# Performance work log

Measured on AMD Instinct MI355X. Metric: run time of the kernel, lower is better.

Reference implementation:

```python
import jax, jax.numpy as jnp
import numpy as np

N_FFT = 4096
HOP = 1024
WIN = 300          # wiener_win_len (frames per independent Wiener chunk)
EPS = 1e-10
SCALE_FACTOR = 10.0


def hann(n):
    # torch.hann_window (periodic)
    return 0.5 * (1.0 - jnp.cos(2.0 * jnp.pi * jnp.arange(n) / n))


def stft(x, window):
    # x: (N, C, T) -> complex (N, C, B, F), center=True, reflect pad, onesided
    pad = N_FFT // 2
    xp = jnp.pad(x, ((0, 0), (0, 0), (pad, pad)), mode='reflect')
    n_frames = 1 + (xp.shape[-1] - N_FFT) // HOP
    idx = jnp.arange(n_frames)[:, None] * HOP + jnp.arange(N_FFT)[None, :]
    frames = xp[..., idx] * window                      # (N,C,F,n_fft)
    spec = jnp.fft.rfft(frames, axis=-1)                # (N,C,F,B)
    return jnp.swapaxes(spec, -1, -2)                   # (N,C,B,F)


def istft(spec, window, length):
    # spec: (..., B, F) complex -> (..., length) real; center=True inverse
    frames = jnp.fft.irfft(jnp.swapaxes(spec, -1, -2), n=N_FFT, axis=-1) * window
    n_frames = frames.shape[-2]
    out_len = N_FFT + HOP * (n_frames - 1)
    idx = jnp.arange(n_frames)[:, None] * HOP + jnp.arange(N_FFT)[None, :]
    out = jnp.zeros(frames.shape[:-2] + (out_len,), frames.dtype).at[..., idx].add(frames)
    wsum = jnp.zeros((out_len,), frames.dtype).at[idx].add(
        jnp.broadcast_to(window ** 2, idx.shape))
    out = out / jnp.where(wsum > 1e-11, wsum, 1.0)
    pad = N_FFT // 2
    return out[..., pad:pad + length]


def wiener_chunk(v, x, niter):
    # openunmix.filtering.wiener (softmask=False, residual=False) on one chunk.
    # v: (T, B, C, S) real target magnitudes; x: (T, B, C) complex mix STFT.
    phase = jnp.exp(1j * jnp.angle(x))                  # mixture phase init
    y = (v * phase[..., None]).astype(jnp.complex64)    # (T,B,C,S)
    max_abs = jnp.maximum(1.0, jnp.max(jnp.abs(x)) / SCALE_FACTOR)
    x = x / max_abs
    y = y / max_abs
    C = x.shape[-1]
    reg = np.sqrt(EPS) * jnp.eye(C, dtype=jnp.complex64)
    for _ in range(niter):  # expectation_maximization, one pass per iter
        psd = jnp.mean(jnp.abs(y) ** 2, axis=2)         # (T,B,S) channel-avg PSD
        # spatial covariance per bin/source, normalized by eps + sum_t psd
        R = jnp.einsum('tbcs,tbds->bcds', y, jnp.conj(y))
        R = R / (EPS + jnp.sum(psd, axis=0))[:, None, None, :]
        Cxx = reg + jnp.einsum('tbs,bcds->tbcd', psd.astype(jnp.complex64), R)
        inv = jnp.linalg.inv(Cxx)                       # (T,B,C,C)
        gain = jnp.einsum('bacs,tbcd->tbads', R, inv) * psd[:, :, None, None, :]
        y = jnp.einsum('tbacs,tbc->tbas', gain, x)      # (T,B,C,S)
    return y * max_abs


def setup_inputs() -> dict:
    key = jax.random.key(0)
    k1, k2 = jax.random.split(key)
    audio = jax.random.normal(k1, (2, 2, 613376), dtype=jnp.float32)
    W = jax.random.normal(k2, (4, 2049), dtype=jnp.float32)  # per-target per-bin mask logits
    return {'audio': audio, 'W': W, 'niter': 1}


def reference(audio, W, niter):
    window = hann(N_FFT).astype(audio.dtype)
    mix = stft(audio, window)                           # (N,C,B,F) complex
    X = jnp.abs(mix)                                    # ComplexNorm power=1
    # target models (stand-in: per-bin sigmoid masks); input detached as in torch
    Xd = jax.lax.stop_gradient(X)
    masks = jax.nn.sigmoid(W)                           # (S,B)
    specs = Xd[..., None] * jnp.transpose(masks)[None, None, :, None, :]  # (N,C,B,F,S)
    v = jnp.transpose(specs, (0, 3, 2, 1, 4))           # (N,F,B,C,S)
    xm = jnp.transpose(mix, (0, 3, 2, 1))               # (N,F,B,C)
    N, F, B, C = xm.shape
    S = v.shape[-1]
    n_chunks = F // WIN
    vc = v.reshape(N, n_chunks, WIN, B, C, S)
    xc = xm.reshape(N, n_chunks, WIN, B, C)
    wfun = lambda vv, xx: wiener_chunk(vv, xx, niter)
    yc = jax.vmap(jax.vmap(wfun))(vc, xc)               # (N,chunks,T,B,C,S)
    y = yc.reshape(N, F, B, C, S)
    y = jnp.transpose(y, (0, 4, 3, 2, 1))               # (N,S,C,B,F)
    estimates = istft(y, window, audio.shape[-1])       # (N,S,C,T)
    return estimates
```

## Files before the change

### kernel.cpp

```cpp
#include <hip/hip_runtime.h>
#include <math.h>

#define TLEN 613376
#define OLEN 617472
#define NFR  600
#define NB   2049
#define PI_F  3.14159265358979323846f
#define PI2_F 6.28318530717958647693f
#define PHYS(i) ((i) + ((i) >> 4))

__device__ __forceinline__ float winf(int j) {
  return 0.5f - 0.5f * __cosf(1.5339807878856412e-3f * (float)j);
}

__device__ __forceinline__ float reflect_load(const float* __restrict__ x, int pos) {
  int k = pos - 2048;
  if (k < 0) k = -k;
  else if (k >= TLEN) k = 2 * TLEN - 2 - k;
  return x[k];
}

__device__ __forceinline__ float2 cmul(float2 a, float2 b) {
  return make_float2(a.x * b.x - a.y * b.y, a.x * b.y + a.y * b.x);
}
__device__ __forceinline__ float2 cadd(float2 a, float2 b) { return make_float2(a.x + b.x, a.y + b.y); }
__device__ __forceinline__ float2 csub(float2 a, float2 b) { return make_float2(a.x - b.x, a.y - b.y); }
template<int SGN>
__device__ __forceinline__ float2 muli(float2 a) {
  return (SGN > 0) ? make_float2(-a.y, a.x) : make_float2(a.y, -a.x);
}

template<int SGN>
__device__ __forceinline__ void fft4(float2 v[4]) {
  float2 t0 = cadd(v[0], v[2]), t1 = csub(v[0], v[2]);
  float2 t2 = cadd(v[1], v[3]), t3 = csub(v[1], v[3]);
  float2 it3 = muli<SGN>(t3);
  v[0] = cadd(t0, t2); v[2] = csub(t0, t2);
  v[1] = cadd(t1, it3); v[3] = csub(t1, it3);
}

template<int SGN>
__device__ __forceinline__ void fft8(float2 v[8]) {
  const float C = 0.70710678118654752440f;
  const float s = (SGN > 0) ? 1.0f : -1.0f;
  float2 t0 = cadd(v[0], v[4]), t1 = csub(v[0], v[4]);
  float2 t2 = cadd(v[2], v[6]), t3 = csub(v[2], v[6]);
  float2 e0 = cadd(t0, t2), e2 = csub(t0, t2);
  float2 it3 = muli<SGN>(t3);
  float2 e1 = cadd(t1, it3), e3 = csub(t1, it3);
  t0 = cadd(v[1], v[5]); t1 = csub(v[1], v[5]);
  t2 = cadd(v[3], v[7]); t3 = csub(v[3], v[7]);
  float2 o0 = cadd(t0, t2), o2 = csub(t0, t2);
  it3 = muli<SGN>(t3);
  float2 o1 = cadd(t1, it3), o3 = csub(t1, it3);
  float2 o1w = make_float2(C * (o1.x - s * o1.y), C * (o1.y + s * o1.x));
  float2 o2w = muli<SGN>(o2);
  float2 o3w = make_float2(C * (-o3.x - s * o3.y), C * (-o3.y + s * o3.x));
  v[0] = cadd(e0, o0);  v[4] = csub(e0, o0);
  v[1] = cadd(e1, o1w); v[5] = csub(e1, o1w);
  v[2] = cadd(e2, o2w); v[6] = csub(e2, o2w);
  v[3] = cadd(e3, o3w); v[7] = csub(e3, o3w);
}

template<int SGN>
__device__ __forceinline__ void twiddle8(float2 v[8], float ang) {
  float sn, cs;
  __sincosf((SGN > 0) ? ang : -ang, &sn, &cs);
  float2 w1 = make_float2(cs, sn);
  float2 w = w1;
  v[1] = cmul(v[1], w);
#pragma unroll
  for (int r = 2; r < 8; ++r) { w = cmul(w, w1); v[r] = cmul(v[r], w); }
}

template<int SGN>
__device__ __forceinline__ void fft2048_mid(float2* lds, float2 v[8], int tid) {
  fft8<SGN>(v);
#pragma unroll
  for (int r = 0; r < 8; ++r) { int i = tid * 8 + r; lds[PHYS(i)] = v[r]; }
  __syncthreads();
#pragma unroll
  for (int r = 0; r < 8; ++r) v[r] = lds[PHYS(tid + 256 * r)];
  twiddle8<SGN>(v, PI2_F * (1.0f / 64.0f) * (float)(tid & 7));
  fft8<SGN>(v);
  __syncthreads();
#pragma unroll
  for (int r = 0; r < 8; ++r) { int i = ((tid >> 3) << 6) + (tid & 7) + 8 * r; lds[PHYS(i)] = v[r]; }
  __syncthreads();
#pragma unroll
  for (int r = 0; r < 8; ++r) v[r] = lds[PHYS(tid + 256 * r)];
  twiddle8<SGN>(v, PI2_F * (1.0f / 512.0f) * (float)(tid & 63));
  fft8<SGN>(v);
  __syncthreads();
#pragma unroll
  for (int r = 0; r < 8; ++r) { int i = ((tid >> 6) << 9) + (tid & 63) + 64 * r; lds[PHYS(i)] = v[r]; }
  __syncthreads();
}

template<int SGN>
__device__ __forceinline__ void fft2048_last(const float2* lds, int jj, float2 u[4]) {
#pragma unroll
  for (int r = 0; r < 4; ++r) u[r] = lds[PHYS(jj + 512 * r)];
  float sn, cs;
  float ang = PI2_F * (1.0f / 2048.0f) * (float)jj;
  __sincosf((SGN > 0) ? ang : -ang, &sn, &cs);
  float2 w1 = make_float2(cs, sn);
  float2 w2 = cmul(w1, w1);
  float2 w3 = cmul(w2, w1);
  u[1] = cmul(u[1], w1); u[2] = cmul(u[2], w2); u[3] = cmul(u[3], w3);
  fft4<SGN>(u);
}

__global__ __launch_bounds__(256, 6) void stft_kernel(const float* __restrict__ audio,
                                                      float2* __restrict__ X) {
  __shared__ float2 lds[2176];
  int bid = blockIdx.x;
  int f  = bid % NFR;
  int nc = bid / NFR;
  const float* x = audio + (size_t)nc * TLEN;
  int tid = threadIdx.x;
  int base = f * 1024;
  float2 v[8];
#pragma unroll
  for (int r = 0; r < 8; ++r) {
    int k = tid + 256 * r;
    int j0 = 2 * k;
    v[r] = make_float2(reflect_load(x, base + j0)     * winf(j0),
                       reflect_load(x, base + j0 + 1) * winf(j0 + 1));
  }
  fft2048_mid<-1>(lds, v, tid);
  fft2048_last<-1>(lds, tid,        v);
  fft2048_last<-1>(lds, tid + 256,  v + 4);
  __syncthreads();
#pragma unroll
  for (int r = 0; r < 4; ++r) lds[PHYS(tid + 512 * r)] = v[r];
#pragma unroll
  for (int r = 0; r < 4; ++r) lds[PHYS(tid + 256 + 512 * r)] = v[4 + r];
  __syncthreads();
  float2* out = X + (size_t)bid * NB;
  float sn0, cs0;
  __sincosf(-PI_F * (float)tid * (1.0f / 2048.0f), &sn0, &cs0);
  float2 ph = make_float2(cs0, sn0);
  const float2 rot = make_float2(0.92387953251128675613f, -0.38268343236508977173f);
#pragma unroll
  for (int r = 0; r < 9; ++r) {
    int k = tid + 256 * r;
    if (k <= 2048) {
      float2 Zk = lds[PHYS(k & 2047)];
      float2 Zm = lds[PHYS((2048 - k) & 2047)];
      float Ex = 0.5f * (Zk.x + Zm.x), Ey = 0.5f * (Zk.y - Zm.y);
      float Dx = 0.5f * (Zk.x - Zm.x), Dy = 0.5f * (Zk.y + Zm.y);
      float Ox = Dy, Oy = -Dx;
      out[k] = make_float2(Ex + Ox * ph.x - Oy * ph.y, Ey + Ox * ph.y + Oy * ph.x);
    }
    ph = cmul(ph, rot);
  }
}

__global__ __launch_bounds__(256) void maxred_kernel(const float2* __restrict__ X,
                                                     unsigned int* __restrict__ maxsq) {
  __shared__ unsigned int sm;
  if (threadIdx.x == 0) sm = 0u;
  __syncthreads();
  int g = blockIdx.y;
  int n = g >> 1, chunk = g & 1;
  const int len = 300 * NB;
  const float2* p0 = X + ((size_t)(n * 2 + 0) * NFR + chunk * 300) * NB;
  const float2* p1 = X + ((size_t)(n * 2 + 1) * NFR + chunk * 300) * NB;
  float l = 0.f;
  for (int i = blockIdx.x * 256 + threadIdx.x; i < len; i += 64 * 256) {
    float2 a = p0[i]; l = fmaxf(l, a.x * a.x + a.y * a.y);
    float2 b = p1[i]; l = fmaxf(l, b.x * b.x + b.y * b.y);
  }
  atomicMax(&sm, __float_as_uint(l));
  __syncthreads();
  if (threadIdx.x == 0) atomicMax(&maxsq[g], sm);
}

__global__ __launch_bounds__(256) void stats_kernel(const float2* __restrict__ X,
                                                    float* __restrict__ stats) {
  int b = blockIdx.x * 256 + threadIdx.x;
  if (b >= NB) return;
  int g = blockIdx.y;
  int n = g >> 1, chunk = g & 1;
  int t0 = blockIdx.z * 75;
  const float2* X0 = X + ((size_t)(n * 2 + 0) * NFR + chunk * 300 + t0) * NB + b;
  const float2* X1 = X + ((size_t)(n * 2 + 1) * NFR + chunk * 300 + t0) * NB + b;
  float s00 = 0.f, s11 = 0.f, sre = 0.f, sim = 0.f;
  for (int t = 0; t < 75; ++t) {
    float2 a = X0[(size_t)t * NB];
    float2 c = X1[(size_t)t * NB];
    s00 += a.x * a.x + a.y * a.y;
    s11 += c.x * c.x + c.y * c.y;
    sre += a.x * c.x + a.y * c.y;
    sim += a.y * c.x - a.x * c.y;
  }
  unsafeAtomicAdd(&stats[(size_t)(g * 4 + 0) * NB + b], s00);
  unsafeAtomicAdd(&stats[(size_t)(g * 4 + 1) * NB + b], s11);
  unsafeAtomicAdd(&stats[(size_t)(g * 4 + 2) * NB + b], sre);
  unsafeAtomicAdd(&stats[(size_t)(g * 4 + 3) * NB + b], sim);
}

__global__ __launch_bounds__(256) void alpha_kernel(const float* __restrict__ Wmask,
                                                    const float* __restrict__ stats,
                                                    const unsigned int* __restrict__ maxsq,
                                                    float* __restrict__ alpha) {
  int idx = blockIdx.x * 256 + threadIdx.x;
  if (idx >= 4 * 4 * NB) return;
  int b = idx % NB;
  int gs = idx / NB;
  int s = gs & 3;
  int g = gs >> 2;
  float ma2 = fmaxf(1.0f, __uint_as_float(maxsq[g]) * 0.01f);
  float P = 0.5f * (stats[(size_t)(g * 4 + 0) * NB + b] +
                    stats[(size_t)(g * 4 + 1) * NB + b]) / ma2;
  float mv = 1.0f / (1.0f + expf(-Wmask[s * NB + b]));
  float m2 = mv * mv;
  alpha[idx] = (m2 * m2) / (1e-10f + m2 * P);
}

__global__ __launch_bounds__(256) void wiener_kernel(const float2* __restrict__ X,
                                                     const float* __restrict__ stats,
                                                     const float* __restrict__ alpha,
                                                     const unsigned int* __restrict__ maxsq,
                                                     float2* __restrict__ Wc) {
  int idx = blockIdx.x * 256 + threadIdx.x;
  if (idx >= 4 * 300 * NB) return;
  int b = idx % NB;
  int gt = idx / NB;
  int t = gt % 300;
  int g = gt / 300;
  int n = g >> 1, chunk = g & 1;
  int f = chunk * 300 + t;
  float ma2 = fmaxf(1.0f, __uint_as_float(maxsq[g]) * 0.01f);
  float inv_ma2 = 1.0f / ma2;
  float g00 = stats[(size_t)(g * 4 + 0) * NB + b] * inv_ma2;
  float g11 = stats[(size_t)(g * 4 + 1) * NB + b] * inv_ma2;
  float gre = stats[(size_t)(g * 4 + 2) * NB + b] * inv_ma2;
  float gim = stats[(size_t)(g * 4 + 3) * NB + b] * inv_ma2;
  float K = alpha[(size_t)(g * 4 + 0) * NB + b] + alpha[(size_t)(g * 4 + 1) * NB + b] +
            alpha[(size_t)(g * 4 + 2) * NB + b] + alpha[(size_t)(g * 4 + 3) * NB + b];
  float2 x0 = X[((size_t)(n * 2 + 0) * NFR + f) * NB + b];
  float2 x1 = X[((size_t)(n * 2 + 1) * NFR + f) * NB + b];
  float ph = 0.5f * ((x0.x * x0.x + x0.y * x0.y) + (x1.x * x1.x + x1.y * x1.y)) * inv_ma2;
  float pk = ph * K;
  float M00 = 1e-5f + pk * g00;
  float M11 = 1e-5f + pk * g11;
  float Mre = pk * gre, Mim = pk * gim;
  float det = M00 * M11 - (Mre * Mre + Mim * Mim);
  float sc = ph / det;
  float u0x = M11 * x0.x - (Mre * x1.x - Mim * x1.y);
  float u0y = M11 * x0.y - (Mre * x1.y + Mim * x1.x);
  float u1x = M00 * x1.x - (Mre * x0.x + Mim * x0.y);
  float u1y = M00 * x1.y - (Mre * x0.y - Mim * x0.x);
  float w0x = g00 * u0x + (gre * u1x - gim * u1y);
  float w0y = g00 * u0y + (gre * u1y + gim * u1x);
  float w1x = (gre * u0x + gim * u0y) + g11 * u1x;
  float w1y = (gre * u0y - gim * u0x) + g11 * u1y;
  float2* out = Wc + ((size_t)(n * NFR + f) * 2) * NB + b;
  out[0]  = make_float2(w0x * sc, w0y * sc);
  out[NB] = make_float2(w1x * sc, w1y * sc);
}

template<int ADD>
__global__ __launch_bounds__(256, 6) void istft_pass_kernel(const float2* __restrict__ Wc,
                                                            const float* __restrict__ alpha,
                                                            float* __restrict__ accum,
                                                            int pass) {
  __shared__ float2 lds[2176];
  int bid = blockIdx.x;
  int fi = bid % 150;
  int plane = bid / 150;
  int c = plane & 1;
  int s = (plane >> 1) & 3;
  int n = plane >> 3;
  int f = 4 * fi + pass;
  int g = n * 2 + (f >= 300 ? 1 : 0);
  int tid = threadIdx.x;
  const float2* Wrow = Wc + ((size_t)(n * NFR + f) * 2 + c) * NB;
  const float*  arow = alpha + (size_t)(g * 4 + s) * NB;
  float2 v[8];
  float sn0, cs0;
  __sincosf(PI_F * (float)tid * (1.0f / 2048.0f), &sn0, &cs0);
  float2 ph = make_float2(cs0, sn0);
  const float2 rot = make_float2(0.92387953251128675613f, 0.38268343236508977173f);
#pragma unroll
  for (int r = 0; r < 8; ++r) {
    int k = tid + 256 * r;
    float ak = arow[k];
    float2 sk = Wrow[k]; sk.x *= ak; sk.y *= ak;
    int rk = 2048 - k;
    float am = arow[rk];
    float2 sv = Wrow[rk]; sv.x *= am; sv.y *= am;
    float Ex = 0.5f * (sk.x + sv.x), Ey = 0.5f * (sk.y - sv.y);
    float Dx = 0.5f * (sk.x - sv.x), Dy = 0.5f * (sk.y + sv.y);
    float Ox = Dx * ph.x - Dy * ph.y, Oy = Dx * ph.y + Dy * ph.x;
    v[r] = make_float2(Ex - Oy, Ey + Ox);
    ph = cmul(ph, rot);
  }
  fft2048_mid<1>(lds, v, tid);
  float* acc = accum + (size_t)plane * OLEN + (size_t)f * 1024;
  const float scale = 1.0f / 2048.0f;
#pragma unroll
  for (int half = 0; half < 2; ++half) {
    int jj = tid + 256 * half;
    float2 u[4];
    fft2048_last<1>(lds, jj, u);
#pragma unroll
    for (int r = 0; r < 4; ++r) {
      int m = jj + 512 * r;
      int j0 = 2 * m;
      float2 val = make_float2(u[r].x * scale * winf(j0),
                               u[r].y * scale * winf(j0 + 1));
      float2* p = (float2*)&acc[j0];
      if (ADD) { float2 o = *p; val.x += o.x; val.y += o.y; }
      *p = val;
    }
  }
  if (!ADD && fi == 149) {
    float* tail = accum + (size_t)plane * OLEN + 614400;
    for (int i = tid; i < OLEN - 614400; i += 256) tail[i] = 0.f;
  }
}

__global__ __launch_bounds__(256) void finalize_kernel(const float* __restrict__ accum,
                                                       float* __restrict__ out) {
  int i = blockIdx.x * 256 + threadIdx.x;
  if (i >= 16 * TLEN) return;
  int t = i % TLEN;
  int plane = i / TLEN;
  int m = t + 2048;
  int f_max = m >> 10; if (f_max > 599) f_max = 599;
  int f_min = (m - 3072) >> 10; if (f_min < 0) f_min = 0;
  float ws = 0.f;
  for (int f2 = f_min; f2 <= f_max; ++f2) {
    float w = winf(m - (f2 << 10));
    ws += w * w;
  }
  float denom = (ws > 1e-11f) ? ws : 1.0f;
  out[i] = accum[(size_t)plane * OLEN + m] / denom;
}

extern "C" void kernel_launch(void* const* d_in, const int* in_sizes, int n_in,
                              void* d_out, int out_size, void* d_ws, size_t ws_size,
                              hipStream_t stream) {
  const float* audio = (const float*)d_in[0];
  const float* Wmask = (const float*)d_in[1];
  float* out = (float*)d_out;

  char* ws = (char*)d_ws;
  const size_t off_stats = 0;
  const size_t off_maxsq = 131328;
  const size_t zero_span = off_maxsq + 256;
  const size_t off_accum = zero_span;
  const size_t off_X     = off_accum + 39518208;
  const size_t off_Wc    = off_X + 39340800;
  const size_t off_alpha = off_Wc + 39340800;

  float*        stats = (float*)(ws + off_stats);
  unsigned int* maxsq = (unsigned int*)(ws + off_maxsq);
  float*        accum = (float*)(ws + off_accum);
  float2*       X     = (float2*)(ws + off_X);
  float2*       Wc    = (float2*)(ws + off_Wc);
  float*        alpha = (float*)(ws + off_alpha);

  hipMemsetAsync(ws, 0, zero_span, stream);

  stft_kernel<<<2400, 256, 0, stream>>>(audio, X);
  maxred_kernel<<<dim3(64, 4), 256, 0, stream>>>(X, maxsq);
  stats_kernel<<<dim3(9, 4, 4), 256, 0, stream>>>(X, stats);
  alpha_kernel<<<(4 * 4 * NB + 255) / 256, 256, 0, stream>>>(Wmask, stats, maxsq, alpha);
  wiener_kernel<<<(4 * 300 * NB + 255) / 256, 256, 0, stream>>>(X, stats, alpha, maxsq, Wc);
  istft_pass_kernel<0><<<2400, 256, 0, stream>>>(Wc, alpha, accum, 0);
  istft_pass_kernel<1><<<2400, 256, 0, stream>>>(Wc, alpha, accum, 1);
  istft_pass_kernel<1><<<2400, 256, 0, stream>>>(Wc, alpha, accum, 2);
  istft_pass_kernel<1><<<2400, 256, 0, stream>>>(Wc, alpha, accum, 3);
  finalize_kernel<<<(16 * TLEN + 255) / 256, 256, 0, stream>>>(accum, out);
}
```

Baseline: 240.2 us.

## Fuse Wiener filter into iSTFT passes and finalize into last pass

Merges the max reduction into the stats kernel and precomputes per-bin alpha sums. The Wiener gain is now computed on the fly inside each iSTFT pass and staged in LDS, so the large Wc intermediate is no longer written and read back. The final overlap-add normalization is folded into the last pass, which writes the output directly and uses a constant inverse window sum in the interior. This removes three launches and about 40 MB of round-trip traffic, but each of the 16 (source, channel) planes per frame now recomputes the Wiener math from X.

```diff
diff --git a/kernel.cpp b/kernel.cpp
--- a/kernel.cpp
+++ b/kernel.cpp
@@ -11,6 +11,17 @@
 
 __device__ __forceinline__ float winf(int j) {
   return 0.5f - 0.5f * __cosf(1.5339807878856412e-3f * (float)j);
+}
+
+__device__ __forceinline__ float wsum_at(int m) {
+  int f_max = m >> 10; if (f_max > 599) f_max = 599;
+  int f_min = (m - 3072) >> 10; if (f_min < 0) f_min = 0;
+  float ws = 0.f;
+  for (int f2 = f_min; f2 <= f_max; ++f2) {
+    float w = winf(m - (f2 << 10));
+    ws += w * w;
+  }
+  return (ws > 1e-11f) ? ws : 1.0f;
 }
 
 __device__ __forceinline__ float reflect_load(const float* __restrict__ x, int pos) {
@@ -157,115 +168,109 @@
   }
 }
 
-__global__ __launch_bounds__(256) void maxred_kernel(const float2* __restrict__ X,
-                                                     unsigned int* __restrict__ maxsq) {
+__global__ __launch_bounds__(256) void stats_kernel(const float2* __restrict__ X,
+                                                    float* __restrict__ stats4,
+                                                    unsigned int* __restrict__ maxsq) {
   __shared__ unsigned int sm;
   if (threadIdx.x == 0) sm = 0u;
   __syncthreads();
-  int g = blockIdx.y;
-  int n = g >> 1, chunk = g & 1;
-  const int len = 300 * NB;
-  const float2* p0 = X + ((size_t)(n * 2 + 0) * NFR + chunk * 300) * NB;
-  const float2* p1 = X + ((size_t)(n * 2 + 1) * NFR + chunk * 300) * NB;
-  float l = 0.f;
-  for (int i = blockIdx.x * 256 + threadIdx.x; i < len; i += 64 * 256) {
-    float2 a = p0[i]; l = fmaxf(l, a.x * a.x + a.y * a.y);
-    float2 b = p1[i]; l = fmaxf(l, b.x * b.x + b.y * b.y);
-  }
-  atomicMax(&sm, __float_as_uint(l));
-  __syncthreads();
-  if (threadIdx.x == 0) atomicMax(&maxsq[g], sm);
-}
-
-__global__ __launch_bounds__(256) void stats_kernel(const float2* __restrict__ X,
-                                                    float* __restrict__ stats) {
   int b = blockIdx.x * 256 + threadIdx.x;
-  if (b >= NB) return;
+  bool ok = (b < NB);
   int g = blockIdx.y;
   int n = g >> 1, chunk = g & 1;
   int t0 = blockIdx.z * 75;
-  const float2* X0 = X + ((size_t)(n * 2 + 0) * NFR + chunk * 300 + t0) * NB + b;
-  const float2* X1 = X + ((size_t)(n * 2 + 1) * NFR + chunk * 300 + t0) * NB + b;
-  float s00 = 0.f, s11 = 0.f, sre = 0.f, sim = 0.f;
-  for (int t = 0; t < 75; ++t) {
-    float2 a = X0[(size_t)t * NB];
-    float2 c = X1[(size_t)t * NB];
-    s00 += a.x * a.x + a.y * a.y;
-    s11 += c.x * c.x + c.y * c.y;
-    sre += a.x * c.x + a.y * c.y;
-    sim += a.y * c.x - a.x * c.y;
-  }
-  unsafeAtomicAdd(&stats[(size_t)(g * 4 + 0) * NB + b], s00);
-  unsafeAtomicAdd(&stats[(size_t)(g * 4 + 1) * NB + b], s11);
-  unsafeAtomicAdd(&stats[(size_t)(g * 4 + 2) * NB + b], sre);
-  unsafeAtomicAdd(&stats[(size_t)(g * 4 + 3) * NB + b], sim);
+  const float2* X0 = X + ((size_t)(n * 2 + 0) * NFR + chunk * 300 + t0) * NB + (ok ? b : 0);
+  const float2* X1 = X + ((size_t)(n * 2 + 1) * NFR + chunk * 300 + t0) * NB + (ok ? b : 0);
+  float s00 = 0.f, s11 = 0.f, sre = 0.f, sim = 0.f, lmax = 0.f;
+  if (ok) {
+    for (int t = 0; t < 75; ++t) {
+      float2 a = X0[(size_t)t * NB];
+      float2 c = X1[(size_t)t * NB];
+      float pa = a.x * a.x + a.y * a.y;
+      float pc = c.x * c.x + c.y * c.y;
+      s00 += pa; s11 += pc;
+      sre += a.x * c.x + a.y * c.y;
+      sim += a.y * c.x - a.x * c.y;
+      lmax = fmaxf(lmax, fmaxf(pa, pc));
+    }
+  }
+  atomicMax(&sm, __float_as_uint(lmax));
+  __syncthreads();
+  if (threadIdx.x == 0) atomicMax(&maxsq[g], sm);
+  if (ok) {
+    float* sp = stats4 + ((size_t)g * NB + b) * 4;
+    unsafeAtomicAdd(sp + 0, s00);
+    unsafeAtomicAdd(sp + 1, s11);
+    unsafeAtomicAdd(sp + 2, sre);
+    unsafeAtomicAdd(sp + 3, sim);
+  }
 }
 
 __global__ __launch_bounds__(256) void alpha_kernel(const float* __restrict__ Wmask,
-                                                    const float* __restrict__ stats,
+                                                    const float4* __restrict__ stats4,
                                                     const unsigned int* __restrict__ maxsq,
-                                                    float* __restrict__ alpha) {
+                                                    float* __restrict__ alpha,
+                                                    float* __restrict__ Ksum) {
   int idx = blockIdx.x * 256 + threadIdx.x;
-  if (idx >= 4 * 4 * NB) return;
+  if (idx >= 4 * NB) return;
   int b = idx % NB;
-  int gs = idx / NB;
-  int s = gs & 3;
-  int g = gs >> 2;
+  int g = idx / NB;
   float ma2 = fmaxf(1.0f, __uint_as_float(maxsq[g]) * 0.01f);
-  float P = 0.5f * (stats[(size_t)(g * 4 + 0) * NB + b] +
-                    stats[(size_t)(g * 4 + 1) * NB + b]) / ma2;
-  float mv = 1.0f / (1.0f + expf(-Wmask[s * NB + b]));
-  float m2 = mv * mv;
-  alpha[idx] = (m2 * m2) / (1e-10f + m2 * P);
-}
-
-__global__ __launch_bounds__(256) void wiener_kernel(const float2* __restrict__ X,
-                                                     const float* __restrict__ stats,
-                                                     const float* __restrict__ alpha,
-                                                     const unsigned int* __restrict__ maxsq,
-                                                     float2* __restrict__ Wc) {
-  int idx = blockIdx.x * 256 + threadIdx.x;
-  if (idx >= 4 * 300 * NB) return;
-  int b = idx % NB;
-  int gt = idx / NB;
-  int t = gt % 300;
-  int g = gt / 300;
-  int n = g >> 1, chunk = g & 1;
-  int f = chunk * 300 + t;
-  float ma2 = fmaxf(1.0f, __uint_as_float(maxsq[g]) * 0.01f);
-  float inv_ma2 = 1.0f / ma2;
-  float g00 = stats[(size_t)(g * 4 + 0) * NB + b] * inv_ma2;
-  float g11 = stats[(size_t)(g * 4 + 1) * NB + b] * inv_ma2;
-  float gre = stats[(size_t)(g * 4 + 2) * NB + b] * inv_ma2;
-  float gim = stats[(size_t)(g * 4 + 3) * NB + b] * inv_ma2;
-  float K = alpha[(size_t)(g * 4 + 0) * NB + b] + alpha[(size_t)(g * 4 + 1) * NB + b] +
-            alpha[(size_t)(g * 4 + 2) * NB + b] + alpha[(size_t)(g * 4 + 3) * NB + b];
-  float2 x0 = X[((size_t)(n * 2 + 0) * NFR + f) * NB + b];
-  float2 x1 = X[((size_t)(n * 2 + 1) * NFR + f) * NB + b];
-  float ph = 0.5f * ((x0.x * x0.x + x0.y * x0.y) + (x1.x * x1.x + x1.y * x1.y)) * inv_ma2;
+  float4 s4 = stats4[(size_t)g * NB + b];
+  float P = 0.5f * (s4.x + s4.y) / ma2;
+  float K = 0.f;
+#pragma unroll
+  for (int s = 0; s < 4; ++s) {
+    float mv = 1.0f / (1.0f + expf(-Wmask[s * NB + b]));
+    float m2 = mv * mv;
+    float a = (m2 * m2) / (1e-10f + m2 * P);
+    alpha[(size_t)(g * 4 + s) * NB + b] = a;
+    K += a;
+  }
+  Ksum[(size_t)g * NB + b] = K;
+}
+
+__device__ __forceinline__ float2 wiener_eval(int b, const float2* __restrict__ x0row,
+                                              const float2* __restrict__ x1row,
+                                              const float4* __restrict__ srow,
+                                              const float* __restrict__ arow,
+                                              const float* __restrict__ krow,
+                                              float ima2, int c) {
+  float4 s4 = srow[b];
+  float g00 = s4.x * ima2, g11 = s4.y * ima2, gre = s4.z * ima2, gim = s4.w * ima2;
+  float K = krow[b];
+  float as = arow[b];
+  float2 x0 = x0row[b], x1 = x1row[b];
+  float ph = 0.5f * ((x0.x * x0.x + x0.y * x0.y) + (x1.x * x1.x + x1.y * x1.y)) * ima2;
   float pk = ph * K;
   float M00 = 1e-5f + pk * g00;
   float M11 = 1e-5f + pk * g11;
   float Mre = pk * gre, Mim = pk * gim;
   float det = M00 * M11 - (Mre * Mre + Mim * Mim);
-  float sc = ph / det;
+  float sc = ph * as / det;
   float u0x = M11 * x0.x - (Mre * x1.x - Mim * x1.y);
   float u0y = M11 * x0.y - (Mre * x1.y + Mim * x1.x);
   float u1x = M00 * x1.x - (Mre * x0.x + Mim * x0.y);
   float u1y = M00 * x1.y - (Mre * x0.y - Mim * x0.x);
-  float w0x = g00 * u0x + (gre * u1x - gim * u1y);
-  float w0y = g00 * u0y + (gre * u1y + gim * u1x);
-  float w1x = (gre * u0x + gim * u0y) + g11 * u1x;
-  float w1y = (gre * u0y - gim * u0x) + g11 * u1y;
-  float2* out = Wc + ((size_t)(n * NFR + f) * 2) * NB + b;
-  out[0]  = make_float2(w0x * sc, w0y * sc);
-  out[NB] = make_float2(w1x * sc, w1y * sc);
-}
-
-template<int ADD>
-__global__ __launch_bounds__(256, 6) void istft_pass_kernel(const float2* __restrict__ Wc,
+  float wx, wy;
+  if (c == 0) {
+    wx = g00 * u0x + (gre * u1x - gim * u1y);
+    wy = g00 * u0y + (gre * u1y + gim * u1x);
+  } else {
+    wx = (gre * u0x + gim * u0y) + g11 * u1x;
+    wy = (gre * u0y - gim * u0x) + g11 * u1y;
+  }
+  return make_float2(wx * sc, wy * sc);
+}
+
+template<int MODE>
+__global__ __launch_bounds__(256, 6) void istft_pass_kernel(const float2* __restrict__ X,
+                                                            const float4* __restrict__ stats4,
                                                             const float* __restrict__ alpha,
+                                                            const float* __restrict__ Ksum,
+                                                            const unsigned int* __restrict__ maxsq,
                                                             float* __restrict__ accum,
+                                                            float* __restrict__ out,
                                                             int pass) {
   __shared__ float2 lds[2176];
   int bid = blockIdx.x;
@@ -277,8 +282,18 @@
   int f = 4 * fi + pass;
   int g = n * 2 + (f >= 300 ? 1 : 0);
   int tid = threadIdx.x;
-  const float2* Wrow = Wc + ((size_t)(n * NFR + f) * 2 + c) * NB;
+  const float2* x0row = X + ((size_t)(n * 2 + 0) * NFR + f) * NB;
+  const float2* x1row = X + ((size_t)(n * 2 + 1) * NFR + f) * NB;
+  const float4* srow = stats4 + (size_t)g * NB;
   const float*  arow = alpha + (size_t)(g * 4 + s) * NB;
+  const float*  krow = Ksum + (size_t)g * NB;
+  float ima2 = 1.0f / fmaxf(1.0f, __uint_as_float(maxsq[g]) * 0.01f);
+#pragma unroll
+  for (int r = 0; r < 9; ++r) {
+    int k = tid + 256 * r;
+    if (k <= 2048) lds[k] = wiener_eval(k, x0row, x1row, srow, arow, krow, ima2, c);
+  }
+  __syncthreads();
   float2 v[8];
   float sn0, cs0;
   __sincosf(PI_F * (float)tid * (1.0f / 2048.0f), &sn0, &cs0);
@@ -287,19 +302,18 @@
 #pragma unroll
   for (int r = 0; r < 8; ++r) {
     int k = tid + 256 * r;
-    float ak = arow[k];
-    float2 sk = Wrow[k]; sk.x *= ak; sk.y *= ak;
-    int rk = 2048 - k;
-    float am = arow[rk];
-    float2 sv = Wrow[rk]; sv.x *= am; sv.y *= am;
+    float2 sk = lds[k];
+    float2 sv = lds[2048 - k];
     float Ex = 0.5f * (sk.x + sv.x), Ey = 0.5f * (sk.y - sv.y);
     float Dx = 0.5f * (sk.x - sv.x), Dy = 0.5f * (sk.y + sv.y);
     float Ox = Dx * ph.x - Dy * ph.y, Oy = Dx * ph.y + Dy * ph.x;
     v[r] = make_float2(Ex - Oy, Ey + Ox);
     ph = cmul(ph, rot);
   }
+  __syncthreads();
   fft2048_mid<1>(lds, v, tid);
   float* acc = accum + (size_t)plane * OLEN + (size_t)f * 1024;
+  float* outp = out + (size_t)plane * TLEN;
   const float scale = 1.0f / 2048.0f;
 #pragma unroll
   for (int half = 0; half < 2; ++half) {
@@ -313,32 +327,37 @@
       float2 val = make_float2(u[r].x * scale * winf(j0),
                                u[r].y * scale * winf(j0 + 1));
       float2* p = (float2*)&acc[j0];
-      if (ADD) { float2 o = *p; val.x += o.x; val.y += o.y; }
-      *p = val;
+      if (MODE == 0) {
+        *p = val;
+      } else if (MODE == 1) {
+        float2 o = *p; val.x += o.x; val.y += o.y;
+        *p = val;
+      } else {
+        int gm = f * 1024 + j0;
+        if (gm < 615424) {
+          float2 o = *p; val.x += o.x; val.y += o.y;
+          float i0, i1;
+          if (gm >= 3072 && gm + 1 < 614400) {
+            i0 = 0.66666666666666667f; i1 = i0;
+          } else {
+            i0 = 1.0f / wsum_at(gm); i1 = 1.0f / wsum_at(gm + 1);
+          }
+          float2* po = (float2*)&outp[gm - 2048];
+          *po = make_float2(val.x * i0, val.y * i1);
+        }
+      }
     }
   }
-  if (!ADD && fi == 149) {
+  if (MODE == 0 && fi == 149) {
     float* tail = accum + (size_t)plane * OLEN + 614400;
     for (int i = tid; i < OLEN - 614400; i += 256) tail[i] = 0.f;
   }
-}
-
-__global__ __launch_bounds__(256) void finalize_kernel(const float* __restrict__ accum,
-                                                       float* __restrict__ out) {
-  int i = blockIdx.x * 256 + threadIdx.x;
-  if (i >= 16 * TLEN) return;
-  int t = i % TLEN;
-  int plane = i / TLEN;
-  int m = t + 2048;
-  int f_max = m >> 10; if (f_max > 599) f_max = 599;
-  int f_min = (m - 3072) >> 10; if (f_min < 0) f_min = 0;
-  float ws = 0.f;
-  for (int f2 = f_min; f2 <= f_max; ++f2) {
-    float w = winf(m - (f2 << 10));
-    ws += w * w;
-  }
-  float denom = (ws > 1e-11f) ? ws : 1.0f;
-  out[i] = accum[(size_t)plane * OLEN + m] / denom;
+  if (MODE == 2 && fi == 0) {
+    float* accp = accum + (size_t)plane * OLEN;
+    for (int m = 2048 + tid; m < 3072; m += 256) {
+      outp[m - 2048] = accp[m] / wsum_at(m);
+    }
+  }
 }
 
 extern "C" void kernel_launch(void* const* d_in, const int* in_sizes, int n_in,
@@ -349,31 +368,29 @@
   float* out = (float*)d_out;
 
   char* ws = (char*)d_ws;
-  const size_t off_stats = 0;
-  const size_t off_maxsq = 131328;
-  const size_t zero_span = off_maxsq + 256;
-  const size_t off_accum = zero_span;
-  const size_t off_X     = off_accum + 39518208;
-  const size_t off_Wc    = off_X + 39340800;
-  const size_t off_alpha = off_Wc + 39340800;
-
-  float*        stats = (float*)(ws + off_stats);
-  unsigned int* maxsq = (unsigned int*)(ws + off_maxsq);
-  float*        accum = (float*)(ws + off_accum);
-  float2*       X     = (float2*)(ws + off_X);
-  float2*       Wc    = (float2*)(ws + off_Wc);
-  float*        alpha = (float*)(ws + off_alpha);
+  const size_t off_stats4 = 0;
+  const size_t off_maxsq  = 131136;
+  const size_t zero_span  = 131200;
+  const size_t off_X      = zero_span;
+  const size_t off_accum  = off_X + 39340800;
+  const size_t off_alpha  = off_accum + 39518208;
+  const size_t off_Ksum   = off_alpha + 131136;
+
+  float*        stats4f = (float*)(ws + off_stats4);
+  float4*       stats4  = (float4*)(ws + off_stats4);
+  unsigned int* maxsq   = (unsigned int*)(ws + off_maxsq);
+  float2*       X       = (float2*)(ws + off_X);
+  float*        accum   = (float*)(ws + off_accum);
+  float*        alpha   = (float*)(ws + off_alpha);
+  float*        Ksum    = (float*)(ws + off_Ksum);
 
   hipMemsetAsync(ws, 0, zero_span, stream);
 
   stft_kernel<<<2400, 256, 0, stream>>>(audio, X);
-  maxred_kernel<<<dim3(64, 4), 256, 0, stream>>>(X, maxsq);
-  stats_kernel<<<dim3(9, 4, 4), 256, 0, stream>>>(X, stats);
-  alpha_kernel<<<(4 * 4 * NB + 255) / 256, 256, 0, stream>>>(Wmask, stats, maxsq, alpha);
-  wiener_kernel<<<(4 * 300 * NB + 255) / 256, 256, 0, stream>>>(X, stats, alpha, maxsq, Wc);
-  istft_pass_kernel<0><<<2400, 256, 0, stream>>>(Wc, alpha, accum, 0);
-  istft_pass_kernel<1><<<2400, 256, 0, stream>>>(Wc, alpha, accum, 1);
-  istft_pass_kernel<1><<<2400, 256, 0, stream>>>(Wc, alpha, accum, 2);
-  istft_pass_kernel<1><<<2400, 256, 0, stream>>>(Wc, alpha, accum, 3);
-  finalize_kernel<<<(16 * TLEN + 255) / 256, 256, 0, stream>>>(accum, out);
-}
+  stats_kernel<<<dim3(9, 4, 4), 256, 0, stream>>>(X, stats4f, maxsq);
+  alpha_kernel<<<(4 * NB + 255) / 256, 256, 0, stream>>>(Wmask, stats4, maxsq, alpha, Ksum);
+  istft_pass_kernel<0><<<2400, 256, 0, stream>>>(X, stats4, alpha, Ksum, maxsq, accum, out, 0);
+  istft_pass_kernel<1><<<2400, 256, 0, stream>>>(X, stats4, alpha, Ksum, maxsq, accum, out, 1);
+  istft_pass_kernel<1><<<2400, 256, 0, stream>>>(X, stats4, alpha, Ksum, maxsq, accum, out, 2);
+  istft_pass_kernel<2><<<2400, 256, 0, stream>>>(X, stats4, alpha, Ksum, maxsq, accum, out, 3);
+}
```

New measurement: 220.2 us. -8.3%, faster.
